# Performance work log

Hardware: AMD Instinct MI355X
Metric: run time of the kernel (lower is better)

## Reference

```python
import jax, jax.numpy as jnp
import numpy as np

B, N, D = 512, 8, 2048
NP = N * (N - 1)  # number of ordered pairs


def _mlp2(h, w0, b0, w1, b1):
    # Linear -> ReLU -> Linear -> ReLU (matches Sequential with one extra layer)
    h = jax.nn.relu(h @ w0 + b0)
    return jax.nn.relu(h @ w1 + b1)


def setup_inputs() -> dict:
    key = jax.random.key(0)
    ks = jax.random.split(key, 10)
    s = 0.02
    x = jax.random.normal(ks[0], (B, N, D), dtype=jnp.float32)
    # structured pair index: for each object i, its N-1 neighbors j (j != i), col2 = valid flag
    pairs = np.array([(i, j, 1) for i in range(N) for j in range(N) if j != i], dtype=np.int32)
    g_idx = jnp.asarray(np.broadcast_to(pairs[None], (B, NP, 3)).copy())
    def w(k, shape):
        return jax.random.normal(k, shape, dtype=jnp.float32) * s
    return {
        "x": x, "g_idx": g_idx,
        "sd_w0": w(ks[1], (D, D)), "sd_b0": jnp.zeros((D,), jnp.float32),
        "sd_w1": w(ks[2], (D, D)), "sd_b1": jnp.zeros((D,), jnp.float32),
        "rd_w0": w(ks[3], (2 * D, D)), "rd_b0": jnp.zeros((D,), jnp.float32),
        "rd_w1": w(ks[4], (D, D)), "rd_b1": jnp.zeros((D,), jnp.float32),
        "af_w0": w(ks[5], (D, D)), "af_b0": jnp.zeros((D,), jnp.float32),
        "af_w1": w(ks[6], (D, D)), "af_b1": jnp.zeros((D,), jnp.float32),
        "ag_w0": w(ks[7], (2 * D, D)), "ag_b0": jnp.zeros((D,), jnp.float32),
        "ag_w1": w(ks[8], (D, D)), "ag_b1": jnp.zeros((D,), jnp.float32),
    }


def reference(x, g_idx, sd_w0, sd_b0, sd_w1, sd_b1, rd_w0, rd_b0, rd_w1, rd_b1,
              af_w0, af_b0, af_w1, af_b1, ag_w0, ag_b0, ag_w1, ag_b1):
    b, n, d = x.shape
    s = x
    # x1 = x.repeat(1, n-1, 1): row k of x1 equals x[:, k % n]
    x1 = jnp.tile(x, (1, n - 1, 1))                      # [B, N*(N-1), D]
    y1 = jnp.take_along_axis(x1, g_idx[..., 0:1], axis=1)  # [B, NP, D]
    y2 = jnp.take_along_axis(x1, g_idx[..., 1:2], axis=1)
    r = jnp.concatenate([y1, y2], axis=-1) * g_idx[:, :, 2:3].astype(x.dtype)  # [B, NP, 2D]
    r = r.reshape(b, n, n - 1, 2 * d)
    r = _mlp2(r, rd_w0, rd_b0, rd_w1, rd_b1)             # [B, N, N-1, D]
    r = r.sum(axis=2)                                    # [B, N, D]
    xs = _mlp2(x, sd_w0, sd_b0, sd_w1, sd_b1)            # [B, N, D]
    pred = xs + r
    a = _mlp2(pred, af_w0, af_b0, af_w1, af_b1)
    a = jnp.concatenate([a, s], axis=2)                  # [B, N, 2D]
    out = _mlp2(a, ag_w0, ag_b0, ag_w1, ag_b1)           # [B, N, D]
    return out
```

## Files before the change

### kernel.cpp

```cpp
#include <hip/hip_runtime.h>
#include <hip/hip_bf16.h>

typedef __bf16 bf16_t;
typedef __bf16 bf16x8 __attribute__((ext_vector_type(8)));
typedef float f32x4 __attribute__((ext_vector_type(4)));

#define DEVINL static __device__ __forceinline__

DEVINL void gload_lds16(const void* g, void* l) {
  __builtin_amdgcn_global_load_lds(
      (__attribute__((address_space(1))) void*)g,
      (__attribute__((address_space(3))) void*)l, 16, 0, 0);
}

struct Prep { const float* s[10]; bf16_t* d[10]; int ld[10]; const float* x; bf16_t* xb; };
__global__ __launch_bounds__(256) void k_prep(Prep a) {
  if (blockIdx.z == 10) {
    int t = (blockIdx.y * 64 + blockIdx.x) * 256 + threadIdx.x;
    const float4* p = (const float4*)a.x + (size_t)t * 2;
    float4 u = p[0], v = p[1];
    bf16x8 o;
    o[0] = (bf16_t)u.x; o[1] = (bf16_t)u.y; o[2] = (bf16_t)u.z; o[3] = (bf16_t)u.w;
    o[4] = (bf16_t)v.x; o[5] = (bf16_t)v.y; o[6] = (bf16_t)v.z; o[7] = (bf16_t)v.w;
    *(bf16x8*)(a.xb + (size_t)t * 8) = o;
    return;
  }
  __shared__ float tile[32][33];
  const int z = blockIdx.z;
  const float* W = a.s[z];
  bf16_t* WT = a.d[z];
  const int dld = a.ld[z];
  int tx = threadIdx.x & 31, ty = threadIdx.x >> 5;
  int n0 = blockIdx.x * 32, k0 = blockIdx.y * 32;
  #pragma unroll
  for (int i = 0; i < 32; i += 8)
    tile[ty + i][tx] = W[(size_t)(k0 + ty + i) * 2048 + n0 + tx];
  __syncthreads();
  #pragma unroll
  for (int i = 0; i < 32; i += 8)
    WT[(size_t)(n0 + ty + i) * dld + k0 + tx] = (bf16_t)tile[tx][ty + i];
}

__global__ __launch_bounds__(256) void k_h1(const bf16_t* __restrict__ uv, int ldu,
                                            int uo, int vo,
                                            const float* __restrict__ b0,
                                            bf16_t* __restrict__ h1, int pbase) {
  int pl = blockIdx.x;
  int c0 = threadIdx.x * 8;
  int p = pbase + pl;
  int b = p >> 6, q = p & 63;
  int i = q >> 3, jj = q & 7;
  if (jj == 7) {
    bf16x8 z = {};
    *(bf16x8*)(h1 + (size_t)pl * 2048 + c0) = z;
    return;
  }
  int j = jj + (jj >= i ? 1 : 0);
  bf16x8 u = *(const bf16x8*)(uv + (size_t)(b * 8 + i) * ldu + uo + c0);
  bf16x8 v = *(const bf16x8*)(uv + (size_t)(b * 8 + j) * ldu + vo + c0);
  const float4* bp = (const float4*)(b0 + c0);
  float4 ba = bp[0], bb4 = bp[1];
  float bb[8] = {ba.x, ba.y, ba.z, ba.w, bb4.x, bb4.y, bb4.z, bb4.w};
  bf16x8 h;
  #pragma unroll
  for (int e = 0; e < 8; ++e)
    h[e] = (bf16_t)fmaxf((float)u[e] + (float)v[e] + bb[e], 0.f);
  *(bf16x8*)(h1 + (size_t)pl * 2048 + c0) = h;
}

template <typename TOUT, int BM, int BN, int NW, int MODE>
__global__ __launch_bounds__(NW * 64, 2) void k_gemm(
    const bf16_t* __restrict__ A, const bf16_t* __restrict__ A2, int lda, int ksplit,
    const bf16_t* __restrict__ BT, int ldb,
    const float* __restrict__ bias, int act_ncol,
    TOUT* __restrict__ C, int N, int K,
    const bf16_t* __restrict__ xsp, int drow) {
  constexpr int WN = NW / 2;
  constexpr int MF = BM / 32;
  constexpr int MH = MF / 2;
  constexpr int NF = BN / (16 * WN);
  static_assert(NF == 4, "engine assumes 4 B-fragments per wave");
  constexpr int AQ = BM / (16 * NW);
  constexpr int BQ = BN / (16 * NW);
  constexpr int AHALF = BM * 64;
  constexpr int BHALF = BN * 64;
  constexpr int AREG = 2 * AHALF;
  constexpr int BUFS = AREG + 2 * BHALF;
  constexpr int NWAIT = AQ + 2 * BQ;

  extern __shared__ char smem[];
  const int t = threadIdx.x;
  const int w = t >> 6, l = t & 63;

  const int nwg = gridDim.x * gridDim.y;
  const int bid = blockIdx.y * gridDim.x + blockIdx.x;
  const int q8 = nwg >> 3, r8 = nwg & 7, xcd = bid & 7, sidx = bid >> 3;
  const int wg = (xcd < r8 ? xcd * (q8 + 1) : r8 * (q8 + 1) + (xcd - r8) * q8) + sidx;
  const int NB = gridDim.x;
  int mb, nb;
  if (((NB & 1) | (nwg & 3) | ((nwg / NB) & 1)) == 0) {
    int wg2 = wg >> 2, r2 = wg & 3, sc = NB >> 1;
    mb = (wg2 / sc) * 2 + (r2 >> 1);
    nb = (wg2 % sc) * 2 + (r2 & 1);
  } else {
    mb = wg / NB; nb = wg % NB;
  }
  const int m0 = mb * BM, n0 = nb * BN;

  size_t Aoffq[AQ], Boffq[BQ];
  #pragma unroll
  for (int q = 0; q < AQ; ++q) {
    int r = w * (BM / NW) + q * 16 + (l >> 2);
    int sq = (((l & 3) ^ ((r >> 1) & 3))) * 8;
    Aoffq[q] = (size_t)(m0 + r) * lda + sq;
  }
  #pragma unroll
  for (int q = 0; q < BQ; ++q) {
    int r = w * (BN / NW) + q * 16 + (l >> 2);
    int sq = (((l & 3) ^ ((r >> 1) & 3))) * 8;
    Boffq[q] = (size_t)(n0 + r) * ldb + sq;
  }
  const int nkt = K >> 6;

  auto stage = [&](int tau, int buf, int h) {
    const int isA = h & 1, kh = h >> 1;
    char* lb = smem + buf * BUFS + (isA ? kh * AHALF : AREG + kh * BHALF) +
               w * (isA ? (AHALF / NW) : (BHALF / NW));
    const int kk = tau * 64 + kh * 32;
    if (isA) {
      const bf16_t* Ab = A;
      int sub = 0;
      if (A2 != nullptr && tau * 64 >= ksplit) { Ab = A2; sub = ksplit; }
      #pragma unroll
      for (int q = 0; q < AQ; ++q)
        gload_lds16(Ab + Aoffq[q] + (kk - sub), lb + q * 1024);
    } else {
      #pragma unroll
      for (int q = 0; q < BQ; ++q)
        gload_lds16(BT + Boffq[q] + kk, lb + q * 1024);
    }
  };

  const int wm = w / WN, wn = w % WN;
  const int lr = l & 15, lg = l >> 4;
  int aoff[MF], boff[NF];
  #pragma unroll
  for (int mf = 0; mf < MF; ++mf) {
    int r = wm * (BM / 2) + mf * 16 + lr;
    aoff[mf] = r * 64 + ((lg ^ ((r >> 1) & 3)) << 4);
  }
  #pragma unroll
  for (int nf = 0; nf < NF; ++nf) {
    int r = wn * 64 + nf * 16 + lr;
    boff[nf] = AREG + r * 64 + ((lg ^ ((r >> 1) & 3)) << 4);
  }

  f32x4 acc[MF][NF] = {};

  #pragma unroll
  for (int h = 0; h < 4; ++h) stage(0, 0, h);
  {
    int t1 = nkt > 1 ? 1 : 0;
    stage(t1, 1, 0); stage(t1, 1, 1); stage(t1, 1, 2);
  }
  if constexpr (NWAIT == 6) asm volatile("s_waitcnt vmcnt(6)");
  else                      asm volatile("s_waitcnt vmcnt(5)");
  __builtin_amdgcn_sched_barrier(0);
  __builtin_amdgcn_s_barrier();

  auto tile_body = [&](int tile, int buf) {
    char* base = smem + buf * BUFS;
    const int tn1 = (tile + 1 < nkt) ? tile + 1 : nkt - 1;
    const int tn2 = (tile + 2 < nkt) ? tile + 2 : nkt - 1;
    bf16x8 af[MH], bfr[NF];

    #pragma unroll
    for (int nf = 0; nf < NF; ++nf) bfr[nf] = *(const bf16x8*)(base + boff[nf]);
    #pragma unroll
    for (int mf = 0; mf < MH; ++mf) af[mf] = *(const bf16x8*)(base + aoff[mf]);
    stage(tn1, buf ^ 1, 3);
    __builtin_amdgcn_s_setprio(1);
    #pragma unroll
    for (int mf = 0; mf < MH; ++mf)
      #pragma unroll
      for (int nf = 0; nf < NF; ++nf)
        acc[mf][nf] = __builtin_amdgcn_mfma_f32_16x16x32_bf16(af[mf], bfr[nf], acc[mf][nf], 0, 0, 0);
    __builtin_amdgcn_s_setprio(0);
    __builtin_amdgcn_sched_barrier(0);
    __builtin_amdgcn_s_barrier();

    #pragma unroll
    for (int mf = 0; mf < MH; ++mf) af[mf] = *(const bf16x8*)(base + aoff[MH + mf]);
    stage(tn2, buf, 0);
    __builtin_amdgcn_s_setprio(1);
    #pragma unroll
    for (int mf = 0; mf < MH; ++mf)
      #pragma unroll
      for (int nf = 0; nf < NF; ++nf)
        acc[MH + mf][nf] = __builtin_amdgcn_mfma_f32_16x16x32_bf16(af[mf], bfr[nf], acc[MH + mf][nf], 0, 0, 0);
    __builtin_amdgcn_s_setprio(0);
    __builtin_amdgcn_sched_barrier(0);
    __builtin_amdgcn_s_barrier();

    #pragma unroll
    for (int nf = 0; nf < NF; ++nf) bfr[nf] = *(const bf16x8*)(base + BHALF + boff[nf]);
    #pragma unroll
    for (int mf = 0; mf < MH; ++mf) af[mf] = *(const bf16x8*)(base + AHALF + aoff[mf]);
    stage(tn2, buf, 1);
    __builtin_amdgcn_s_setprio(1);
    #pragma unroll
    for (int mf = 0; mf < MH; ++mf)
      #pragma unroll
      for (int nf = 0; nf < NF; ++nf)
        acc[mf][nf] = __builtin_amdgcn_mfma_f32_16x16x32_bf16(af[mf], bfr[nf], acc[mf][nf], 0, 0, 0);
    __builtin_amdgcn_s_setprio(0);
    __builtin_amdgcn_sched_barrier(0);
    __builtin_amdgcn_s_barrier();

    #pragma unroll
    for (int mf = 0; mf < MH; ++mf) af[mf] = *(const bf16x8*)(base + AHALF + aoff[MH + mf]);
    stage(tn2, buf, 2);
    __builtin_amdgcn_s_setprio(1);
    #pragma unroll
    for (int mf = 0; mf < MH; ++mf)
      #pragma unroll
      for (int nf = 0; nf < NF; ++nf)
        acc[MH + mf][nf] = __builtin_amdgcn_mfma_f32_16x16x32_bf16(af[mf], bfr[nf], acc[MH + mf][nf], 0, 0, 0);
    __builtin_amdgcn_s_setprio(0);
    __builtin_amdgcn_sched_barrier(0);
    if constexpr (NWAIT == 6) asm volatile("s_waitcnt vmcnt(6)");
    else                      asm volatile("s_waitcnt vmcnt(5)");
    __builtin_amdgcn_s_barrier();
  };

  for (int tt = 0; tt < nkt; tt += 2) {
    tile_body(tt, 0);
    tile_body(tt + 1, 1);
  }
  asm volatile("s_waitcnt vmcnt(0)");

  if constexpr (MODE == 1) {
    const int g = lg >> 1;
    const bool hi = (lg & 1) != 0;
    #pragma unroll
    for (int mf = 0; mf < MF; ++mf) {
      #pragma unroll
      for (int nf = 0; nf < NF; ++nf) {
        int col = n0 + wn * 64 + nf * 16 + lr;
        float bv = bias[col];
        float s = fmaxf(acc[mf][nf][0] + bv, 0.f) +
                  fmaxf(acc[mf][nf][1] + bv, 0.f) +
                  fmaxf(acc[mf][nf][2] + bv, 0.f);
        if (!hi) s += fmaxf(acc[mf][nf][3] + bv, 0.f);
        s += __shfl_xor(s, 16, 64);
        if (!hi) {
          int d = drow + (m0 >> 3) + wm * (BM >> 4) + mf * 2 + g;
          float xv = (float)xsp[(size_t)d * N + col];
          C[(size_t)d * N + col] = (TOUT)(xv + s);
        }
      }
    }
  } else {
    #pragma unroll
    for (int mf = 0; mf < MF; ++mf) {
      #pragma unroll
      for (int nf = 0; nf < NF; ++nf) {
        int col = n0 + wn * 64 + nf * 16 + lr;
        bool act = col < act_ncol;
        float bv = act ? bias[col] : 0.f;
        #pragma unroll
        for (int ri = 0; ri < 4; ++ri) {
          int row = m0 + wm * (BM / 2) + mf * 16 + lg * 4 + ri;
          float v = acc[mf][nf][ri] + bv;
          if (act) v = fmaxf(v, 0.f);
          C[(size_t)row * N + col] = (TOUT)v;
        }
      }
    }
  }
}

extern "C" void kernel_launch(void* const* d_in, const int* in_sizes, int n_in,
                              void* d_out, int out_size, void* d_ws, size_t ws_size,
                              hipStream_t stream) {
  const float* x     = (const float*)d_in[0];
  const float* sd_w0 = (const float*)d_in[2];
  const float* sd_b0 = (const float*)d_in[3];
  const float* sd_w1 = (const float*)d_in[4];
  const float* sd_b1 = (const float*)d_in[5];
  const float* rd_w0 = (const float*)d_in[6];
  const float* rd_b0 = (const float*)d_in[7];
  const float* rd_w1 = (const float*)d_in[8];
  const float* rd_b1 = (const float*)d_in[9];
  const float* af_w0 = (const float*)d_in[10];
  const float* af_b0 = (const float*)d_in[11];
  const float* af_w1 = (const float*)d_in[12];
  const float* af_b1 = (const float*)d_in[13];
  const float* ag_w0 = (const float*)d_in[14];
  const float* ag_b0 = (const float*)d_in[15];
  const float* ag_w1 = (const float*)d_in[16];
  const float* ag_b1 = (const float*)d_in[17];
  float* out = (float*)d_out;

  const int D = 2048, M = 4096;
  const size_t DD = (size_t)D * D;
  const size_t MN = (size_t)M * D;
  const int MCP = 16384;
  const size_t LDS256 = 131072, LDS128 = 98304;

  hipFuncSetAttribute((const void*)k_gemm<bf16_t, 256, 256, 8, 1>,
                      hipFuncAttributeMaxDynamicSharedMemorySize, (int)LDS256);
  hipFuncSetAttribute((const void*)k_gemm<bf16_t, 128, 256, 8, 0>,
                      hipFuncAttributeMaxDynamicSharedMemorySize, (int)LDS256);
  hipFuncSetAttribute((const void*)k_gemm<float, 128, 256, 8, 0>,
                      hipFuncAttributeMaxDynamicSharedMemorySize, (int)LDS256);

  char* wp = (char*)d_ws;
  auto alloc = [&](size_t bytes) -> void* {
    void* p = (void*)wp;
    wp += (bytes + 255) & ~(size_t)255;
    return p;
  };
  bf16_t* xb    = (bf16_t*)alloc(MN * 2);
  bf16_t* wcat  = (bf16_t*)alloc((size_t)3 * DD * 2);
  bf16_t* sdw1T = (bf16_t*)alloc(DD * 2);
  bf16_t* rdw1T = (bf16_t*)alloc(DD * 2);
  bf16_t* afw0T = (bf16_t*)alloc(DD * 2);
  bf16_t* afw1T = (bf16_t*)alloc(DD * 2);
  bf16_t* agw0T = (bf16_t*)alloc(DD * 4);
  bf16_t* agw1T = (bf16_t*)alloc(DD * 2);
  bf16_t* tuv   = (bf16_t*)alloc(MN * 3 * 2);
  bf16_t* xs    = (bf16_t*)alloc(MN * 2);
  const size_t used0 = (size_t)(wp - (char*)d_ws);
  const size_t h1big = (size_t)2 * MCP * D * 2;
  const size_t h1sm  = (size_t)MCP * D * 2;
  const bool big = ws_size >= used0 + h1big + MN * 2 + 1024;
  bf16_t* h1c   = (bf16_t*)alloc(big ? h1big : h1sm);
  bf16_t* predb = (bf16_t*)alloc(MN * 2);
  (void)in_sizes; (void)n_in; (void)out_size;

  bf16_t* S1 = h1c;
  bf16_t* S2 = h1c + MN;

  Prep tp;
  tp.s[0] = sd_w0;           tp.d[0] = wcat;            tp.ld[0] = D;
  tp.s[1] = rd_w0;           tp.d[1] = wcat + DD;       tp.ld[1] = D;
  tp.s[2] = rd_w0 + DD;      tp.d[2] = wcat + 2 * DD;   tp.ld[2] = D;
  tp.s[3] = sd_w1;           tp.d[3] = sdw1T;           tp.ld[3] = D;
  tp.s[4] = rd_w1;           tp.d[4] = rdw1T;           tp.ld[4] = D;
  tp.s[5] = af_w0;           tp.d[5] = afw0T;           tp.ld[5] = D;
  tp.s[6] = af_w1;           tp.d[6] = afw1T;           tp.ld[6] = D;
  tp.s[7] = ag_w1;           tp.d[7] = agw1T;           tp.ld[7] = D;
  tp.s[8] = ag_w0;           tp.d[8] = agw0T;           tp.ld[8] = 2 * D;
  tp.s[9] = ag_w0 + DD;      tp.d[9] = agw0T + D;       tp.ld[9] = 2 * D;
  tp.x = x; tp.xb = xb;
  k_prep<<<dim3(64, 64, 11), 256, 0, stream>>>(tp);

  dim3 g128(D / 256, M / 128);

  k_gemm<bf16_t, 128, 256, 8, 0><<<dim3(24, 32), 512, LDS128, stream>>>(
      xb, nullptr, D, 0, wcat, D, sd_b0, D, tuv, 3 * D, D, nullptr, 0);
  k_gemm<bf16_t, 128, 256, 8, 0><<<g128, 512, LDS128, stream>>>(
      tuv, nullptr, 3 * D, 0, sdw1T, D, sd_b1, D, xs, D, D, nullptr, 0);

  if (big) {
    k_h1<<<dim3(2 * MCP), 256, 0, stream>>>(tuv, 3 * D, D, 2 * D, rd_b0, h1c, 0);
    k_gemm<bf16_t, 256, 256, 8, 1><<<dim3(D / 256, 2 * MCP / 256), 512, LDS256, stream>>>(
        h1c, nullptr, D, 0, rdw1T, D, rd_b1, D, predb, D, D, xs, 0);
  } else {
    for (int c = 0; c < 2; ++c) {
      k_h1<<<dim3(MCP), 256, 0, stream>>>(tuv, 3 * D, D, 2 * D, rd_b0, h1c, c * MCP);
      k_gemm<bf16_t, 256, 256, 8, 1><<<dim3(D / 256, MCP / 256), 512, LDS256, stream>>>(
          h1c, nullptr, D, 0, rdw1T, D, rd_b1, D, predb, D, D, xs, c * 2048);
    }
  }

  k_gemm<bf16_t, 128, 256, 8, 0><<<g128, 512, LDS128, stream>>>(
      predb, nullptr, D, 0, afw0T, D, af_b0, D, S1, D, D, nullptr, 0);
  k_gemm<bf16_t, 128, 256, 8, 0><<<g128, 512, LDS128, stream>>>(
      S1, nullptr, D, 0, afw1T, D, af_b1, D, S2, D, D, nullptr, 0);
  k_gemm<bf16_t, 128, 256, 8, 0><<<g128, 512, LDS128, stream>>>(
      S2, xb, D, D, agw0T, 2 * D, ag_b0, D, S1, D, 2 * D, nullptr, 0);
  k_gemm<float, 128, 256, 8, 0><<<g128, 512, LDS128, stream>>>(
      S1, nullptr, D, 0, agw1T, D, ag_b1, D, out, D, D, nullptr, 0);
}
```

Measured before the change: 698.6 us.

## Switch GEMM engine to 32x32x16 MFMA fragments and always chunk pair GEMM

Rewrites the GEMM inner loop to use 32x32x16 bf16 MFMA instructions instead of 16x16x32, with new LDS fragment offsets and new epilogue row mappings for both the plain and pair-sum modes. The larger MFMA tile is meant to raise math throughput per LDS read and cut instruction count. It also drops the single big pair-GEMM path and always processes the pair MLP in two chunks, which shrinks workspace but adds extra launches. The new accumulator layout makes the epilogue stores more scattered.

```diff
diff --git a/kernel.cpp b/kernel.cpp
--- a/kernel.cpp
+++ b/kernel.cpp
@@ -3,7 +3,7 @@
 
 typedef __bf16 bf16_t;
 typedef __bf16 bf16x8 __attribute__((ext_vector_type(8)));
-typedef float f32x4 __attribute__((ext_vector_type(4)));
+typedef float f32x16 __attribute__((ext_vector_type(16)));
 
 #define DEVINL static __device__ __forceinline__
 
@@ -76,10 +76,11 @@
     TOUT* __restrict__ C, int N, int K,
     const bf16_t* __restrict__ xsp, int drow) {
   constexpr int WN = NW / 2;
-  constexpr int MF = BM / 32;
-  constexpr int MH = MF / 2;
-  constexpr int NF = BN / (16 * WN);
-  static_assert(NF == 4, "engine assumes 4 B-fragments per wave");
+  constexpr int RF = BM / 64;
+  constexpr int RH = RF / 2;
+  static_assert(RH >= 1, "BM too small");
+  constexpr int NF = BN / (32 * WN);
+  static_assert(NF == 2, "engine assumes 2 B-fragments (64 cols) per wave");
   constexpr int AQ = BM / (16 * NW);
   constexpr int BQ = BN / (16 * NW);
   constexpr int AHALF = BM * 64;
@@ -142,20 +143,24 @@
   };
 
   const int wm = w / WN, wn = w % WN;
-  const int lr = l & 15, lg = l >> 4;
-  int aoff[MF], boff[NF];
-  #pragma unroll
-  for (int mf = 0; mf < MF; ++mf) {
-    int r = wm * (BM / 2) + mf * 16 + lr;
-    aoff[mf] = r * 64 + ((lg ^ ((r >> 1) & 3)) << 4);
+  const int lc = l & 31, hi = l >> 5;
+  int aoff[RF][2], boff[NF][2];
+  #pragma unroll
+  for (int rf = 0; rf < RF; ++rf) {
+    int r = wm * (BM / 2) + rf * 32 + lc;
+    #pragma unroll
+    for (int ks = 0; ks < 2; ++ks)
+      aoff[rf][ks] = r * 64 + ((((ks * 2 + hi)) ^ ((r >> 1) & 3)) << 4);
   }
   #pragma unroll
   for (int nf = 0; nf < NF; ++nf) {
-    int r = wn * 64 + nf * 16 + lr;
-    boff[nf] = AREG + r * 64 + ((lg ^ ((r >> 1) & 3)) << 4);
-  }
-
-  f32x4 acc[MF][NF] = {};
+    int r = wn * 64 + nf * 32 + lc;
+    #pragma unroll
+    for (int ks = 0; ks < 2; ++ks)
+      boff[nf][ks] = AREG + r * 64 + ((((ks * 2 + hi)) ^ ((r >> 1) & 3)) << 4);
+  }
+
+  f32x16 acc[RF][NF] = {};
 
   #pragma unroll
   for (int h = 0; h < 4; ++h) stage(0, 0, h);
@@ -172,60 +177,86 @@
     char* base = smem + buf * BUFS;
     const int tn1 = (tile + 1 < nkt) ? tile + 1 : nkt - 1;
     const int tn2 = (tile + 2 < nkt) ? tile + 2 : nkt - 1;
-    bf16x8 af[MH], bfr[NF];
-
-    #pragma unroll
-    for (int nf = 0; nf < NF; ++nf) bfr[nf] = *(const bf16x8*)(base + boff[nf]);
-    #pragma unroll
-    for (int mf = 0; mf < MH; ++mf) af[mf] = *(const bf16x8*)(base + aoff[mf]);
+    bf16x8 af[RH][2], bfr[NF][2];
+
+    #pragma unroll
+    for (int nf = 0; nf < NF; ++nf)
+      #pragma unroll
+      for (int ks = 0; ks < 2; ++ks)
+        bfr[nf][ks] = *(const bf16x8*)(base + boff[nf][ks]);
+    #pragma unroll
+    for (int rh = 0; rh < RH; ++rh)
+      #pragma unroll
+      for (int ks = 0; ks < 2; ++ks)
+        af[rh][ks] = *(const bf16x8*)(base + aoff[rh][ks]);
     stage(tn1, buf ^ 1, 3);
     __builtin_amdgcn_s_setprio(1);
     #pragma unroll
-    for (int mf = 0; mf < MH; ++mf)
-      #pragma unroll
-      for (int nf = 0; nf < NF; ++nf)
-        acc[mf][nf] = __builtin_amdgcn_mfma_f32_16x16x32_bf16(af[mf], bfr[nf], acc[mf][nf], 0, 0, 0);
+    for (int ks = 0; ks < 2; ++ks)
+      #pragma unroll
+      for (int rh = 0; rh < RH; ++rh)
+        #pragma unroll
+        for (int nf = 0; nf < NF; ++nf)
+          acc[rh][nf] = __builtin_amdgcn_mfma_f32_32x32x16_bf16(af[rh][ks], bfr[nf][ks], acc[rh][nf], 0, 0, 0);
     __builtin_amdgcn_s_setprio(0);
     __builtin_amdgcn_sched_barrier(0);
     __builtin_amdgcn_s_barrier();
 
     #pragma unroll
-    for (int mf = 0; mf < MH; ++mf) af[mf] = *(const bf16x8*)(base + aoff[MH + mf]);
+    for (int rh = 0; rh < RH; ++rh)
+      #pragma unroll
+      for (int ks = 0; ks < 2; ++ks)
+        af[rh][ks] = *(const bf16x8*)(base + aoff[RH + rh][ks]);
     stage(tn2, buf, 0);
     __builtin_amdgcn_s_setprio(1);
     #pragma unroll
-    for (int mf = 0; mf < MH; ++mf)
-      #pragma unroll
-      for (int nf = 0; nf < NF; ++nf)
-        acc[MH + mf][nf] = __builtin_amdgcn_mfma_f32_16x16x32_bf16(af[mf], bfr[nf], acc[MH + mf][nf], 0, 0, 0);
+    for (int ks = 0; ks < 2; ++ks)
+      #pragma unroll
+      for (int rh = 0; rh < RH; ++rh)
+        #pragma unroll
+        for (int nf = 0; nf < NF; ++nf)
+          acc[RH + rh][nf] = __builtin_amdgcn_mfma_f32_32x32x16_bf16(af[rh][ks], bfr[nf][ks], acc[RH + rh][nf], 0, 0, 0);
     __builtin_amdgcn_s_setprio(0);
     __builtin_amdgcn_sched_barrier(0);
     __builtin_amdgcn_s_barrier();
 
     #pragma unroll
-    for (int nf = 0; nf < NF; ++nf) bfr[nf] = *(const bf16x8*)(base + BHALF + boff[nf]);
-    #pragma unroll
-    for (int mf = 0; mf < MH; ++mf) af[mf] = *(const bf16x8*)(base + AHALF + aoff[mf]);
+    for (int nf = 0; nf < NF; ++nf)
+      #pragma unroll
+      for (int ks = 0; ks < 2; ++ks)
+        bfr[nf][ks] = *(const bf16x8*)(base + BHALF + boff[nf][ks]);
+    #pragma unroll
+    for (int rh = 0; rh < RH; ++rh)
+      #pragma unroll
+      for (int ks = 0; ks < 2; ++ks)
+        af[rh][ks] = *(const bf16x8*)(base + AHALF + aoff[rh][ks]);
     stage(tn2, buf, 1);
     __builtin_amdgcn_s_setprio(1);
     #pragma unroll
-    for (int mf = 0; mf < MH; ++mf)
-      #pragma unroll
-      for (int nf = 0; nf < NF; ++nf)
-        acc[mf][nf] = __builtin_amdgcn_mfma_f32_16x16x32_bf16(af[mf], bfr[nf], acc[mf][nf], 0, 0, 0);
+    for (int ks = 0; ks < 2; ++ks)
+      #pragma unroll
+      for (int rh = 0; rh < RH; ++rh)
+        #pragma unroll
+        for (int nf = 0; nf < NF; ++nf)
+          acc[rh][nf] = __builtin_amdgcn_mfma_f32_32x32x16_bf16(af[rh][ks], bfr[nf][ks], acc[rh][nf], 0, 0, 0);
     __builtin_amdgcn_s_setprio(0);
     __builtin_amdgcn_sched_barrier(0);
     __builtin_amdgcn_s_barrier();
 
     #pragma unroll
-    for (int mf = 0; mf < MH; ++mf) af[mf] = *(const bf16x8*)(base + AHALF + aoff[MH + mf]);
+    for (int rh = 0; rh < RH; ++rh)
+      #pragma unroll
+      for (int ks = 0; ks < 2; ++ks)
+        af[rh][ks] = *(const bf16x8*)(base + AHALF + aoff[RH + rh][ks]);
     stage(tn2, buf, 2);
     __builtin_amdgcn_s_setprio(1);
     #pragma unroll
-    for (int mf = 0; mf < MH; ++mf)
-      #pragma unroll
-      for (int nf = 0; nf < NF; ++nf)
-        acc[MH + mf][nf] = __builtin_amdgcn_mfma_f32_16x16x32_bf16(af[mf], bfr[nf], acc[MH + mf][nf], 0, 0, 0);
+    for (int ks = 0; ks < 2; ++ks)
+      #pragma unroll
+      for (int rh = 0; rh < RH; ++rh)
+        #pragma unroll
+        for (int nf = 0; nf < NF; ++nf)
+          acc[RH + rh][nf] = __builtin_amdgcn_mfma_f32_32x32x16_bf16(af[rh][ks], bfr[nf][ks], acc[RH + rh][nf], 0, 0, 0);
     __builtin_amdgcn_s_setprio(0);
     __builtin_amdgcn_sched_barrier(0);
     if constexpr (NWAIT == 6) asm volatile("s_waitcnt vmcnt(6)");
@@ -240,38 +271,39 @@
   asm volatile("s_waitcnt vmcnt(0)");
 
   if constexpr (MODE == 1) {
-    const int g = lg >> 1;
-    const bool hi = (lg & 1) != 0;
-    #pragma unroll
-    for (int mf = 0; mf < MF; ++mf) {
+    #pragma unroll
+    for (int rf = 0; rf < RF; ++rf) {
       #pragma unroll
       for (int nf = 0; nf < NF; ++nf) {
-        int col = n0 + wn * 64 + nf * 16 + lr;
+        int col = n0 + wn * 64 + nf * 32 + lc;
         float bv = bias[col];
-        float s = fmaxf(acc[mf][nf][0] + bv, 0.f) +
-                  fmaxf(acc[mf][nf][1] + bv, 0.f) +
-                  fmaxf(acc[mf][nf][2] + bv, 0.f);
-        if (!hi) s += fmaxf(acc[mf][nf][3] + bv, 0.f);
-        s += __shfl_xor(s, 16, 64);
-        if (!hi) {
-          int d = drow + (m0 >> 3) + wm * (BM >> 4) + mf * 2 + g;
-          float xv = (float)xsp[(size_t)d * N + col];
-          C[(size_t)d * N + col] = (TOUT)(xv + s);
+        #pragma unroll
+        for (int q = 0; q < 4; ++q) {
+          float s = fmaxf(acc[rf][nf][4 * q + 0] + bv, 0.f) +
+                    fmaxf(acc[rf][nf][4 * q + 1] + bv, 0.f) +
+                    fmaxf(acc[rf][nf][4 * q + 2] + bv, 0.f);
+          if (!hi) s += fmaxf(acc[rf][nf][4 * q + 3] + bv, 0.f);
+          s += __shfl_xor(s, 32, 64);
+          if (!hi) {
+            int d = drow + (m0 >> 3) + wm * (BM >> 4) + rf * 4 + q;
+            float xv = (float)xsp[(size_t)d * N + col];
+            C[(size_t)d * N + col] = (TOUT)(xv + s);
+          }
         }
       }
     }
   } else {
     #pragma unroll
-    for (int mf = 0; mf < MF; ++mf) {
+    for (int rf = 0; rf < RF; ++rf) {
       #pragma unroll
       for (int nf = 0; nf < NF; ++nf) {
-        int col = n0 + wn * 64 + nf * 16 + lr;
+        int col = n0 + wn * 64 + nf * 32 + lc;
         bool act = col < act_ncol;
         float bv = act ? bias[col] : 0.f;
         #pragma unroll
-        for (int ri = 0; ri < 4; ++ri) {
-          int row = m0 + wm * (BM / 2) + mf * 16 + lg * 4 + ri;
-          float v = acc[mf][nf][ri] + bv;
+        for (int r = 0; r < 16; ++r) {
+          int row = m0 + wm * (BM / 2) + rf * 32 + (r & 3) + 8 * (r >> 2) + 4 * hi;
+          float v = acc[rf][nf][r] + bv;
           if (act) v = fmaxf(v, 0.f);
           C[(size_t)row * N + col] = (TOUT)v;
         }
@@ -331,13 +363,9 @@
   bf16_t* agw1T = (bf16_t*)alloc(DD * 2);
   bf16_t* tuv   = (bf16_t*)alloc(MN * 3 * 2);
   bf16_t* xs    = (bf16_t*)alloc(MN * 2);
-  const size_t used0 = (size_t)(wp - (char*)d_ws);
-  const size_t h1big = (size_t)2 * MCP * D * 2;
-  const size_t h1sm  = (size_t)MCP * D * 2;
-  const bool big = ws_size >= used0 + h1big + MN * 2 + 1024;
-  bf16_t* h1c   = (bf16_t*)alloc(big ? h1big : h1sm);
+  bf16_t* h1c   = (bf16_t*)alloc((size_t)MCP * D * 2);
   bf16_t* predb = (bf16_t*)alloc(MN * 2);
-  (void)in_sizes; (void)n_in; (void)out_size;
+  (void)ws_size; (void)in_sizes; (void)n_in; (void)out_size;
 
   bf16_t* S1 = h1c;
   bf16_t* S2 = h1c + MN;
@@ -363,16 +391,10 @@
   k_gemm<bf16_t, 128, 256, 8, 0><<<g128, 512, LDS128, stream>>>(
       tuv, nullptr, 3 * D, 0, sdw1T, D, sd_b1, D, xs, D, D, nullptr, 0);
 
-  if (big) {
-    k_h1<<<dim3(2 * MCP), 256, 0, stream>>>(tuv, 3 * D, D, 2 * D, rd_b0, h1c, 0);
-    k_gemm<bf16_t, 256, 256, 8, 1><<<dim3(D / 256, 2 * MCP / 256), 512, LDS256, stream>>>(
-        h1c, nullptr, D, 0, rdw1T, D, rd_b1, D, predb, D, D, xs, 0);
-  } else {
-    for (int c = 0; c < 2; ++c) {
-      k_h1<<<dim3(MCP), 256, 0, stream>>>(tuv, 3 * D, D, 2 * D, rd_b0, h1c, c * MCP);
-      k_gemm<bf16_t, 256, 256, 8, 1><<<dim3(D / 256, MCP / 256), 512, LDS256, stream>>>(
-          h1c, nullptr, D, 0, rdw1T, D, rd_b1, D, predb, D, D, xs, c * 2048);
-    }
+  for (int c = 0; c < 2; ++c) {
+    k_h1<<<dim3(MCP), 256, 0, stream>>>(tuv, 3 * D, D, 2 * D, rd_b0, h1c, c * MCP);
+    k_gemm<bf16_t, 256, 256, 8, 1><<<dim3(D / 256, MCP / 256), 512, LDS256, stream>>>(
+        h1c, nullptr, D, 0, rdw1T, D, rd_b1, D, predb, D, D, xs, c * 2048);
   }
 
   k_gemm<bf16_t, 128, 256, 8, 0><<<g128, 512, LDS128, stream>>>(
```

After: 742.1 us. 6.2% more time.

## Fuse pair-hidden construction into the relation GEMM A-operand load

Applied to the files above, without the earlier changes.

Removes the separate k_h1 kernel that materialized the 32768x2048 pair hidden tensor. The relation GEMM now gathers u and v rows from the first-layer output and computes relu(u+v) in registers, writing the result straight into LDS. To make that possible, rd_b0 is folded into the first GEMM's epilogue through a concatenated bias (new MODE 2). This saves a large HBM write and re-read, at the cost of register-staged A loads that replace the async global-to-LDS path and add extra synchronization inside the pipeline.

```diff
diff --git a/kernel.cpp b/kernel.cpp
--- a/kernel.cpp
+++ b/kernel.cpp
@@ -13,10 +13,13 @@
       (__attribute__((address_space(3))) void*)l, 16, 0, 0);
 }
 
-struct Prep { const float* s[10]; bf16_t* d[10]; int ld[10]; const float* x; bf16_t* xb; };
+struct Prep { const float* s[10]; bf16_t* d[10]; int ld[10];
+              const float* x; bf16_t* xb;
+              const float* b0a; const float* b0b; float* catb; };
 __global__ __launch_bounds__(256) void k_prep(Prep a) {
   if (blockIdx.z == 10) {
     int t = (blockIdx.y * 64 + blockIdx.x) * 256 + threadIdx.x;
+    if (t < 4096) a.catb[t] = t < 2048 ? a.b0a[t] : a.b0b[t - 2048];
     const float4* p = (const float4*)a.x + (size_t)t * 2;
     float4 u = p[0], v = p[1];
     bf16x8 o;
@@ -41,33 +44,6 @@
     WT[(size_t)(n0 + ty + i) * dld + k0 + tx] = (bf16_t)tile[tx][ty + i];
 }
 
-__global__ __launch_bounds__(256) void k_h1(const bf16_t* __restrict__ uv, int ldu,
-                                            int uo, int vo,
-                                            const float* __restrict__ b0,
-                                            bf16_t* __restrict__ h1, int pbase) {
-  int pl = blockIdx.x;
-  int c0 = threadIdx.x * 8;
-  int p = pbase + pl;
-  int b = p >> 6, q = p & 63;
-  int i = q >> 3, jj = q & 7;
-  if (jj == 7) {
-    bf16x8 z = {};
-    *(bf16x8*)(h1 + (size_t)pl * 2048 + c0) = z;
-    return;
-  }
-  int j = jj + (jj >= i ? 1 : 0);
-  bf16x8 u = *(const bf16x8*)(uv + (size_t)(b * 8 + i) * ldu + uo + c0);
-  bf16x8 v = *(const bf16x8*)(uv + (size_t)(b * 8 + j) * ldu + vo + c0);
-  const float4* bp = (const float4*)(b0 + c0);
-  float4 ba = bp[0], bb4 = bp[1];
-  float bb[8] = {ba.x, ba.y, ba.z, ba.w, bb4.x, bb4.y, bb4.z, bb4.w};
-  bf16x8 h;
-  #pragma unroll
-  for (int e = 0; e < 8; ++e)
-    h[e] = (bf16_t)fmaxf((float)u[e] + (float)v[e] + bb[e], 0.f);
-  *(bf16x8*)(h1 + (size_t)pl * 2048 + c0) = h;
-}
-
 template <typename TOUT, int BM, int BN, int NW, int MODE>
 __global__ __launch_bounds__(NW * 64, 2) void k_gemm(
     const bf16_t* __restrict__ A, const bf16_t* __restrict__ A2, int lda, int ksplit,
@@ -75,6 +51,7 @@
     const float* __restrict__ bias, int act_ncol,
     TOUT* __restrict__ C, int N, int K,
     const bf16_t* __restrict__ xsp, int drow) {
+  constexpr bool FUSE = (MODE == 1);
   constexpr int WN = NW / 2;
   constexpr int MF = BM / 32;
   constexpr int MH = MF / 2;
@@ -107,12 +84,15 @@
   }
   const int m0 = mb * BM, n0 = nb * BN;
 
-  size_t Aoffq[AQ], Boffq[BQ];
-  #pragma unroll
-  for (int q = 0; q < AQ; ++q) {
-    int r = w * (BM / NW) + q * 16 + (l >> 2);
-    int sq = (((l & 3) ^ ((r >> 1) & 3))) * 8;
-    Aoffq[q] = (size_t)(m0 + r) * lda + sq;
+  size_t Aoffq[AQ] = {};
+  size_t Boffq[BQ];
+  if constexpr (!FUSE) {
+    #pragma unroll
+    for (int q = 0; q < AQ; ++q) {
+      int r = w * (BM / NW) + q * 16 + (l >> 2);
+      int sq = (((l & 3) ^ ((r >> 1) & 3))) * 8;
+      Aoffq[q] = (size_t)(m0 + r) * lda + sq;
+    }
   }
   #pragma unroll
   for (int q = 0; q < BQ; ++q) {
@@ -121,6 +101,48 @@
     Boffq[q] = (size_t)(n0 + r) * ldb + sq;
   }
   const int nkt = K >> 6;
+
+  const bf16_t* uB[AQ]; const bf16_t* vB[AQ]; bool vld[AQ]; int wofs[AQ];
+  if constexpr (FUSE) {
+    #pragma unroll
+    for (int q = 0; q < AQ; ++q) {
+      int r = w * (BM / NW) + q * 16 + (l >> 2);
+      int p = m0 + r;
+      int bq = p >> 6, q6 = p & 63, i = q6 >> 3, jj = q6 & 7;
+      vld[q] = (jj != 7);
+      int j = jj + (jj >= i ? 1 : 0);
+      int sq = (((l & 3) ^ ((r >> 1) & 3))) * 8;
+      uB[q] = A + (size_t)(bq * 8 + i) * lda + 2048 + sq;
+      vB[q] = A + (size_t)(bq * 8 + j) * lda + 4096 + sq;
+      wofs[q] = w * (AHALF / NW) + q * 1024 + l * 16;
+    }
+  }
+  struct AR { bf16x8 u[AQ], v[AQ]; };
+  auto loadA = [&](int tau, int kh) {
+    AR ar;
+    #pragma unroll
+    for (int q = 0; q < AQ; ++q) {
+      if (vld[q]) {
+        int c = tau * 64 + kh * 32;
+        ar.u[q] = *(const bf16x8*)(uB[q] + c);
+        ar.v[q] = *(const bf16x8*)(vB[q] + c);
+      } else {
+        ar.u[q] = bf16x8{}; ar.v[q] = bf16x8{};
+      }
+    }
+    return ar;
+  };
+  auto writeA = [&](const AR& ar, int buf, int kh) {
+    #pragma unroll
+    for (int q = 0; q < AQ; ++q) {
+      bf16x8 h;
+      #pragma unroll
+      for (int e = 0; e < 8; ++e)
+        h[e] = (bf16_t)fmaxf((float)ar.u[q][e] + (float)ar.v[q][e], 0.f);
+      *(bf16x8*)(smem + buf * BUFS + kh * AHALF + wofs[q]) = h;
+    }
+  };
+  AR pend;
 
   auto stage = [&](int tau, int buf, int h) {
     const int isA = h & 1, kh = h >> 1;
@@ -157,28 +179,46 @@
 
   f32x4 acc[MF][NF] = {};
 
-  #pragma unroll
-  for (int h = 0; h < 4; ++h) stage(0, 0, h);
-  {
+  if constexpr (FUSE) {
+    stage(0, 0, 0);
+    AR a00 = loadA(0, 0);
+    stage(0, 0, 2);
+    AR a01 = loadA(0, 1);
     int t1 = nkt > 1 ? 1 : 0;
-    stage(t1, 1, 0); stage(t1, 1, 1); stage(t1, 1, 2);
-  }
-  if constexpr (NWAIT == 6) asm volatile("s_waitcnt vmcnt(6)");
-  else                      asm volatile("s_waitcnt vmcnt(5)");
-  __builtin_amdgcn_sched_barrier(0);
-  __builtin_amdgcn_s_barrier();
+    stage(t1, 1, 0);
+    pend = loadA(t1, 0);
+    stage(t1, 1, 2);
+    writeA(a00, 0, 0);
+    writeA(a01, 0, 1);
+    asm volatile("s_waitcnt lgkmcnt(0)" ::: "memory");
+    __builtin_amdgcn_sched_barrier(0);
+    __builtin_amdgcn_s_barrier();
+  } else {
+    #pragma unroll
+    for (int h = 0; h < 4; ++h) stage(0, 0, h);
+    {
+      int t1 = nkt > 1 ? 1 : 0;
+      stage(t1, 1, 0); stage(t1, 1, 1); stage(t1, 1, 2);
+    }
+    if constexpr (NWAIT == 6) asm volatile("s_waitcnt vmcnt(6)");
+    else                      asm volatile("s_waitcnt vmcnt(5)");
+    __builtin_amdgcn_sched_barrier(0);
+    __builtin_amdgcn_s_barrier();
+  }
 
   auto tile_body = [&](int tile, int buf) {
     char* base = smem + buf * BUFS;
     const int tn1 = (tile + 1 < nkt) ? tile + 1 : nkt - 1;
     const int tn2 = (tile + 2 < nkt) ? tile + 2 : nkt - 1;
     bf16x8 af[MH], bfr[NF];
+    AR ak1;
 
     #pragma unroll
     for (int nf = 0; nf < NF; ++nf) bfr[nf] = *(const bf16x8*)(base + boff[nf]);
     #pragma unroll
     for (int mf = 0; mf < MH; ++mf) af[mf] = *(const bf16x8*)(base + aoff[mf]);
-    stage(tn1, buf ^ 1, 3);
+    if constexpr (FUSE) ak1 = loadA(tn1, 1);
+    else                stage(tn1, buf ^ 1, 3);
     __builtin_amdgcn_s_setprio(1);
     #pragma unroll
     for (int mf = 0; mf < MH; ++mf)
@@ -186,6 +226,7 @@
       for (int nf = 0; nf < NF; ++nf)
         acc[mf][nf] = __builtin_amdgcn_mfma_f32_16x16x32_bf16(af[mf], bfr[nf], acc[mf][nf], 0, 0, 0);
     __builtin_amdgcn_s_setprio(0);
+    if constexpr (FUSE) writeA(pend, buf ^ 1, 0);
     __builtin_amdgcn_sched_barrier(0);
     __builtin_amdgcn_s_barrier();
 
@@ -206,7 +247,8 @@
     for (int nf = 0; nf < NF; ++nf) bfr[nf] = *(const bf16x8*)(base + BHALF + boff[nf]);
     #pragma unroll
     for (int mf = 0; mf < MH; ++mf) af[mf] = *(const bf16x8*)(base + AHALF + aoff[mf]);
-    stage(tn2, buf, 1);
+    if constexpr (FUSE) pend = loadA(tn2, 0);
+    else                stage(tn2, buf, 1);
     __builtin_amdgcn_s_setprio(1);
     #pragma unroll
     for (int mf = 0; mf < MH; ++mf)
@@ -214,6 +256,7 @@
       for (int nf = 0; nf < NF; ++nf)
         acc[mf][nf] = __builtin_amdgcn_mfma_f32_16x16x32_bf16(af[mf], bfr[nf], acc[mf][nf], 0, 0, 0);
     __builtin_amdgcn_s_setprio(0);
+    if constexpr (FUSE) writeA(ak1, buf ^ 1, 1);
     __builtin_amdgcn_sched_barrier(0);
     __builtin_amdgcn_s_barrier();
 
@@ -227,9 +270,13 @@
       for (int nf = 0; nf < NF; ++nf)
         acc[MH + mf][nf] = __builtin_amdgcn_mfma_f32_16x16x32_bf16(af[mf], bfr[nf], acc[MH + mf][nf], 0, 0, 0);
     __builtin_amdgcn_s_setprio(0);
-    __builtin_amdgcn_sched_barrier(0);
-    if constexpr (NWAIT == 6) asm volatile("s_waitcnt vmcnt(6)");
-    else                      asm volatile("s_waitcnt vmcnt(5)");
+    if constexpr (FUSE) {
+      asm volatile("s_waitcnt lgkmcnt(0)" ::: "memory");
+    } else {
+      if constexpr (NWAIT == 6) asm volatile("s_waitcnt vmcnt(6)");
+      else                      asm volatile("s_waitcnt vmcnt(5)");
+    }
+    __builtin_amdgcn_sched_barrier(0);
     __builtin_amdgcn_s_barrier();
   };
 
@@ -267,7 +314,9 @@
       for (int nf = 0; nf < NF; ++nf) {
         int col = n0 + wn * 64 + nf * 16 + lr;
         bool act = col < act_ncol;
-        float bv = act ? bias[col] : 0.f;
+        float bv;
+        if constexpr (MODE == 2) bv = (col < 2 * act_ncol) ? bias[col] : 0.f;
+        else                     bv = act ? bias[col] : 0.f;
         #pragma unroll
         for (int ri = 0; ri < 4; ++ri) {
           int row = m0 + wm * (BM / 2) + mf * 16 + lg * 4 + ri;
@@ -305,12 +354,14 @@
   const int D = 2048, M = 4096;
   const size_t DD = (size_t)D * D;
   const size_t MN = (size_t)M * D;
-  const int MCP = 16384;
+  const int MP = 32768;
   const size_t LDS256 = 131072, LDS128 = 98304;
 
   hipFuncSetAttribute((const void*)k_gemm<bf16_t, 256, 256, 8, 1>,
                       hipFuncAttributeMaxDynamicSharedMemorySize, (int)LDS256);
   hipFuncSetAttribute((const void*)k_gemm<bf16_t, 128, 256, 8, 0>,
+                      hipFuncAttributeMaxDynamicSharedMemorySize, (int)LDS256);
+  hipFuncSetAttribute((const void*)k_gemm<bf16_t, 128, 256, 8, 2>,
                       hipFuncAttributeMaxDynamicSharedMemorySize, (int)LDS256);
   hipFuncSetAttribute((const void*)k_gemm<float, 128, 256, 8, 0>,
                       hipFuncAttributeMaxDynamicSharedMemorySize, (int)LDS256);
@@ -329,18 +380,13 @@
   bf16_t* afw1T = (bf16_t*)alloc(DD * 2);
   bf16_t* agw0T = (bf16_t*)alloc(DD * 4);
   bf16_t* agw1T = (bf16_t*)alloc(DD * 2);
+  float*  catb  = (float*)alloc((size_t)2 * D * 4);
   bf16_t* tuv   = (bf16_t*)alloc(MN * 3 * 2);
   bf16_t* xs    = (bf16_t*)alloc(MN * 2);
-  const size_t used0 = (size_t)(wp - (char*)d_ws);
-  const size_t h1big = (size_t)2 * MCP * D * 2;
-  const size_t h1sm  = (size_t)MCP * D * 2;
-  const bool big = ws_size >= used0 + h1big + MN * 2 + 1024;
-  bf16_t* h1c   = (bf16_t*)alloc(big ? h1big : h1sm);
+  bf16_t* S1    = (bf16_t*)alloc(MN * 2);
+  bf16_t* S2    = (bf16_t*)alloc(MN * 2);
   bf16_t* predb = (bf16_t*)alloc(MN * 2);
-  (void)in_sizes; (void)n_in; (void)out_size;
-
-  bf16_t* S1 = h1c;
-  bf16_t* S2 = h1c + MN;
+  (void)ws_size; (void)in_sizes; (void)n_in; (void)out_size;
 
   Prep tp;
   tp.s[0] = sd_w0;           tp.d[0] = wcat;            tp.ld[0] = D;
@@ -354,26 +400,18 @@
   tp.s[8] = ag_w0;           tp.d[8] = agw0T;           tp.ld[8] = 2 * D;
   tp.s[9] = ag_w0 + DD;      tp.d[9] = agw0T + D;       tp.ld[9] = 2 * D;
   tp.x = x; tp.xb = xb;
+  tp.b0a = sd_b0; tp.b0b = rd_b0; tp.catb = catb;
   k_prep<<<dim3(64, 64, 11), 256, 0, stream>>>(tp);
 
   dim3 g128(D / 256, M / 128);
 
-  k_gemm<bf16_t, 128, 256, 8, 0><<<dim3(24, 32), 512, LDS128, stream>>>(
-      xb, nullptr, D, 0, wcat, D, sd_b0, D, tuv, 3 * D, D, nullptr, 0);
+  k_gemm<bf16_t, 128, 256, 8, 2><<<dim3(24, 32), 512, LDS128, stream>>>(
+      xb, nullptr, D, 0, wcat, D, catb, D, tuv, 3 * D, D, nullptr, 0);
   k_gemm<bf16_t, 128, 256, 8, 0><<<g128, 512, LDS128, stream>>>(
       tuv, nullptr, 3 * D, 0, sdw1T, D, sd_b1, D, xs, D, D, nullptr, 0);
 
-  if (big) {
-    k_h1<<<dim3(2 * MCP), 256, 0, stream>>>(tuv, 3 * D, D, 2 * D, rd_b0, h1c, 0);
-    k_gemm<bf16_t, 256, 256, 8, 1><<<dim3(D / 256, 2 * MCP / 256), 512, LDS256, stream>>>(
-        h1c, nullptr, D, 0, rdw1T, D, rd_b1, D, predb, D, D, xs, 0);
-  } else {
-    for (int c = 0; c < 2; ++c) {
-      k_h1<<<dim3(MCP), 256, 0, stream>>>(tuv, 3 * D, D, 2 * D, rd_b0, h1c, c * MCP);
-      k_gemm<bf16_t, 256, 256, 8, 1><<<dim3(D / 256, MCP / 256), 512, LDS256, stream>>>(
-          h1c, nullptr, D, 0, rdw1T, D, rd_b1, D, predb, D, D, xs, c * 2048);
-    }
-  }
+  k_gemm<bf16_t, 256, 256, 8, 1><<<dim3(D / 256, MP / 256), 512, LDS256, stream>>>(
+      tuv, nullptr, 3 * D, 0, rdw1T, D, rd_b1, D, predb, D, D, xs, 0);
 
   k_gemm<bf16_t, 128, 256, 8, 0><<<g128, 512, LDS128, stream>>>(
       predb, nullptr, D, 0, afw0T, D, af_b0, D, S1, D, D, nullptr, 0);
```

New measurement: 861.9 us. 23.4% more time.
